# Kernel tuning notes

Hardware: AMD Instinct MI355X
Metric: run time of the kernel (lower is better)

Reference implementation:

```python
import jax, jax.numpy as jnp
import numpy as np

INP = 64   # inplanes
PLN = 64   # planes
LOC = 64   # loc_planes
EPS = 1e-5


def _linear_init(key, fan_in, fan_out):
    # torch nn.Linear default: U(-1/sqrt(fan_in), 1/sqrt(fan_in)) for W and b
    kw, kb = jax.random.split(key)
    bound = 1.0 / np.sqrt(fan_in)
    W = jax.random.uniform(kw, (fan_in, fan_out), jnp.float32, -bound, bound)
    b = jax.random.uniform(kb, (fan_out,), jnp.float32, -bound, bound)
    return W, b


def setup_inputs() -> dict:
    key = jax.random.key(0)
    ks = jax.random.split(key, 8)
    B, N = 8, 4096
    img_fea = jax.random.normal(ks[0], (B, N, INP), jnp.float32)
    loc_fea = jax.random.normal(ks[1], (B, N, LOC), jnp.float32)
    W11, b11 = _linear_init(ks[2], INP + LOC, INP)
    W12, b12 = _linear_init(ks[3], INP, INP)
    W21, b21 = _linear_init(ks[4], INP + LOC, INP)
    W22, b22 = _linear_init(ks[5], INP, INP * PLN)
    W3, b3 = _linear_init(ks[6], PLN, PLN)
    ln_g = jnp.ones((PLN,), jnp.float32)
    ln_b = jnp.zeros((PLN,), jnp.float32)
    return {
        "img_fea": img_fea, "loc_fea": loc_fea,
        "W11": W11, "b11": b11, "W12": W12, "b12": b12,
        "W21": W21, "b21": b21, "W22": W22, "b22": b22,
        "ln_g": ln_g, "ln_b": ln_b, "W3": W3, "b3": b3,
    }


def reference(img_fea, loc_fea, W11, b11, W12, b12, W21, b21, W22, b22,
              ln_g, ln_b, W3, b3):
    B, N, C = img_fea.shape
    cat_fea = jnp.concatenate([img_fea, loc_fea], axis=2)  # [B,N,INP+LOC]
    # branch 1: per-token input vector
    w11 = jax.nn.relu(cat_fea @ W11 + b11)                 # [B,N,INP]
    w12 = w11 @ W12 + b12                                  # [B,N,INP]
    # branch 2: per-token weight matrix generation
    w21 = jax.nn.relu(cat_fea @ W21 + b21)                 # [B,N,INP]
    w22 = (w21 @ W22 + b22).reshape(B, N, INP, PLN)        # [B,N,INP,PLN]
    # batched tiny matvec: (1,INP) @ (INP,PLN) per token
    x = jnp.einsum('bni,bnio->bno', w12, w22)              # [B,N,PLN]
    # LayerNorm over last dim + ReLU
    mu = jnp.mean(x, axis=-1, keepdims=True)
    var = jnp.mean(jnp.square(x - mu), axis=-1, keepdims=True)
    x = (x - mu) * jax.lax.rsqrt(var + EPS) * ln_g + ln_b
    x = jax.nn.relu(x)
    # final linear (no activation)
    return x @ W3 + b3
```

## Files before the change

### kernel.cpp

```cpp
#include <hip/hip_runtime.h>
#include <cstdint>


typedef __bf16 bf16x4 __attribute__((ext_vector_type(4)));
typedef __bf16 bf16x8 __attribute__((ext_vector_type(8)));
typedef float  f32x4  __attribute__((ext_vector_type(4)));

#define MFMA16(A, B, C) __builtin_amdgcn_mfma_f32_16x16x32_bf16(A, B, C, 0, 0, 0)

#define OFF_BT22 0
#define OFF_W11  266240
#define OFF_W21  274432
#define OFF_W12  282624
#define OFF_W3   286720

__global__ __launch_bounds__(256) void prep_kernel(
    const float* __restrict__ W22, const float* __restrict__ b22,
    const float* __restrict__ W11, const float* __restrict__ W21,
    const float* __restrict__ W12, const float* __restrict__ W3,
    __bf16* __restrict__ ws)
{
    __shared__ __bf16 T[64][72];
    const int b = blockIdx.x, tid = threadIdx.x;
    const float* src; long base = 0;
    if (b < 64)       { src = W22 + b * 4096; }
    else if (b == 64) { src = b22; }
    else if (b < 67)  { src = W11 + (b - 65) * 4096; base = OFF_W11 + (b - 65) * 4096; }
    else if (b < 69)  { src = W21 + (b - 67) * 4096; base = OFF_W21 + (b - 67) * 4096; }
    else if (b == 69) { src = W12;                   base = OFF_W12; }
    else              { src = W3;                    base = OFF_W3; }
    #pragma unroll
    for (int it = 0; it < 4; ++it) {
        int u = it * 1024 + tid * 4;
        int r = u >> 6, c = u & 63;
        const float4 v = *(const float4*)(src + u);
        T[r][c] = (__bf16)v.x; T[r][c + 1] = (__bf16)v.y;
        T[r][c + 2] = (__bf16)v.z; T[r][c + 3] = (__bf16)v.w;
    }
    __syncthreads();
    #pragma unroll
    for (int it = 0; it < 2; ++it) {
        int item = it * 256 + tid;
        int q = item >> 6, o = item & 63;
        bf16x8 pk;
        #pragma unroll
        for (int kj = 0; kj < 8; ++kj) pk[kj] = T[q * 8 + kj][o];
        long dstE;
        if (b <= 64) {
            int k8 = (b == 64 ? 512 : b * 8) + q;
            dstE = OFF_BT22 + ((long)(o >> 4) * 520 + k8) * 128 + (o & 15) * 8;
        } else {
            dstE = base + q * 512 + o * 8;
        }
        *(bf16x8*)(ws + dstE) = pk;
    }
}

#define LOADCH(buf, c) do {                                          \
    buf##_0 = *(const bf16x8*)(Bw + ((c)*16 +  0) * 128);            \
    buf##_1 = *(const bf16x8*)(Bw + ((c)*16 +  4) * 128);            \
    buf##_2 = *(const bf16x8*)(Bw + ((c)*16 +  8) * 128);            \
    buf##_3 = *(const bf16x8*)(Bw + ((c)*16 + 12) * 128);            \
} while (0)

#define COMPUTE_J(b0, b1, j) do {                                    \
    f32x4 w4[4];                                                     \
    _Pragma("unroll")                                                \
    for (int mf = 0; mf < 4; ++mf) {                                 \
        bf16x4 wv4 = *(const bf16x4*)(w21T + (j)*68 + mf*16 + quad*4);\
        w4[mf] = __builtin_convertvector(wv4, f32x4);                \
    }                                                                \
    _Pragma("unroll")                                                \
    for (int mf = 0; mf < 4; ++mf) {                                 \
        f32x4 fz = {};                                               \
        f32x4 m = MFMA16(a12[mf][0], b0, fz);                        \
        m       = MFMA16(a12[mf][1], b1, m);                         \
        _Pragma("unroll")                                            \
        for (int r = 0; r < 4; ++r)                                  \
            acc[mf][r] = fmaf(w4[mf][r], m[r], acc[mf][r]);          \
    }                                                                \
} while (0)

#define COMPUTE(buf, c) do {                                         \
    COMPUTE_J(buf##_0, buf##_1, (c)*2);                              \
    COMPUTE_J(buf##_2, buf##_3, (c)*2 + 1);                          \
} while (0)

__global__ __launch_bounds__(256, 2) void main_kernel(
    const float* __restrict__ img, const float* __restrict__ loc,
    const float* __restrict__ b11, const float* __restrict__ b12,
    const float* __restrict__ b21, const float* __restrict__ ln_g,
    const float* __restrict__ ln_b, const float* __restrict__ b3,
    const __bf16* __restrict__ ws, float* __restrict__ out)
{
    __shared__ __align__(1024) char smem[46592];
    __bf16* catL = (__bf16*)smem;
    __bf16* w11L = (__bf16*)(smem + 17408);
    __bf16* w12L = (__bf16*)(smem + 26624);
    __bf16* w21T = (__bf16*)(smem + 35840);
    float2* ps   = (float2*)(smem + 44544);
    __bf16* xL   = w11L;

    const int tid  = threadIdx.x;
    const int wv   = tid >> 6;
    const int lane = tid & 63;
    const int ln   = lane & 15;
    const int quad = lane >> 4;
    const int ob   = wv * 16;
    const long tb  = (long)blockIdx.x * 64;

    const __bf16* Bt22  = ws + OFF_BT22;
    const __bf16* W11bt = ws + OFF_W11;
    const __bf16* W21bt = ws + OFF_W21;
    const __bf16* W12bt = ws + OFF_W12;
    const __bf16* W3bt  = ws + OFF_W3;

    {
        const float* srcs[2] = {img, loc};
        #pragma unroll
        for (int s = 0; s < 2; ++s) {
            const float* src = srcs[s] + tb * 64;
            #pragma unroll
            for (int it = 0; it < 4; ++it) {
                int u = (it * 256 + tid) * 4;
                int t = u >> 6, c = u & 63;
                const float4 v = *(const float4*)(src + u);
                bf16x4 pk = {(__bf16)v.x, (__bf16)v.y, (__bf16)v.z, (__bf16)v.w};
                *(bf16x4*)(catL + t * 136 + s * 64 + c) = pk;
            }
        }
    }
    __syncthreads();

    {
        const int isW21 = wv >> 1;
        const int cb0 = (wv & 1) * 32;
        const __bf16* Wbt = isW21 ? W21bt : W11bt;
        const float* bsel = isW21 ? b21 : b11;
        f32x4 a1[4][2] = {};
        #pragma unroll
        for (int kb = 0; kb < 4; ++kb) {
            bf16x8 af[4];
            #pragma unroll
            for (int mf = 0; mf < 4; ++mf)
                af[mf] = *(const bf16x8*)(catL + (mf*16 + ln)*136 + kb*32 + quad*8);
            #pragma unroll
            for (int nf = 0; nf < 2; ++nf) {
                bf16x8 bw = *(const bf16x8*)(Wbt + ((kb*4 + quad)*64 + cb0 + nf*16 + ln)*8);
                #pragma unroll
                for (int mf = 0; mf < 4; ++mf)
                    a1[mf][nf] = MFMA16(af[mf], bw, a1[mf][nf]);
            }
        }
        if (!isW21) {
            #pragma unroll
            for (int nf = 0; nf < 2; ++nf) {
                int o = cb0 + nf*16 + ln;
                float cb = bsel[o];
                #pragma unroll
                for (int mf = 0; mf < 4; ++mf)
                    #pragma unroll
                    for (int r = 0; r < 4; ++r) {
                        int t = mf*16 + quad*4 + r;
                        float v = a1[mf][nf][r] + cb; v = v > 0.f ? v : 0.f;
                        w11L[t*72 + o] = (__bf16)v;
                    }
            }
        } else {
            #pragma unroll
            for (int nf = 0; nf < 2; ++nf) {
                int o = cb0 + nf*16 + ln;
                float cb = bsel[o];
                #pragma unroll
                for (int mf = 0; mf < 4; ++mf) {
                    bf16x4 pk;
                    #pragma unroll
                    for (int r = 0; r < 4; ++r) {
                        float v = a1[mf][nf][r] + cb; v = v > 0.f ? v : 0.f;
                        pk[r] = (__bf16)v;
                    }
                    *(bf16x4*)(w21T + o*68 + mf*16 + quad*4) = pk;
                }
            }
        }
    }
    __syncthreads();

    {
        float c12 = b12[ob + ln];
        f32x4 a12c[4] = {};
        #pragma unroll
        for (int kb = 0; kb < 2; ++kb) {
            bf16x8 af[4];
            #pragma unroll
            for (int mf = 0; mf < 4; ++mf)
                af[mf] = *(const bf16x8*)(w11L + (mf*16 + ln)*72 + kb*32 + quad*8);
            bf16x8 bw = *(const bf16x8*)(W12bt + ((kb*4 + quad)*64 + ob + ln)*8);
            #pragma unroll
            for (int mf = 0; mf < 4; ++mf)
                a12c[mf] = MFMA16(af[mf], bw, a12c[mf]);
        }
        #pragma unroll
        for (int mf = 0; mf < 4; ++mf)
            #pragma unroll
            for (int r = 0; r < 4; ++r) {
                int t = mf*16 + quad*4 + r;
                w12L[t*72 + ob + ln] = (__bf16)(a12c[mf][r] + c12);
            }
    }
    __syncthreads();

    bf16x8 a12[4][2];
    #pragma unroll
    for (int mf = 0; mf < 4; ++mf)
        #pragma unroll
        for (int sub = 0; sub < 2; ++sub)
            a12[mf][sub] = *(const bf16x8*)(w12L + (mf*16 + ln)*72 + sub*32 + quad*8);

    const __bf16* Bw = Bt22 + ((long)wv * 520 + quad) * 128 + ln * 8;

    bf16x8 B0_0, B0_1, B0_2, B0_3;
    bf16x8 B1_0, B1_1, B1_2, B1_3;
    bf16x8 B2_0, B2_1, B2_2, B2_3;

    f32x4 acc[4] = {};
    LOADCH(B0, 0); LOADCH(B1, 1);
    #pragma unroll 1
    for (int cc = 0; cc < 32; cc += 3) {
        if (cc + 2 < 32) LOADCH(B2, cc + 2);
        COMPUTE(B0, cc);
        if (cc + 3 < 32) LOADCH(B0, cc + 3);
        if (cc + 1 < 32) COMPUTE(B1, cc + 1);
        if (cc + 4 < 32) LOADCH(B1, cc + 4);
        if (cc + 2 < 32) COMPUTE(B2, cc + 2);
    }
    {
        bf16x8 bb0 = *(const bf16x8*)(Bw + (512 + 0) * 128);
        bf16x8 bb1 = *(const bf16x8*)(Bw + (512 + 4) * 128);
        #pragma unroll
        for (int mf = 0; mf < 4; ++mf) {
            acc[mf] = MFMA16(a12[mf][0], bb0, acc[mf]);
            acc[mf] = MFMA16(a12[mf][1], bb1, acc[mf]);
        }
    }

    #pragma unroll
    for (int mf = 0; mf < 4; ++mf)
        #pragma unroll
        for (int r = 0; r < 4; ++r) {
            float v = acc[mf][r];
            float s1 = v, s2 = v*v;
            #pragma unroll
            for (int d = 1; d < 16; d <<= 1) {
                s1 += __shfl_xor(s1, d, 64);
                s2 += __shfl_xor(s2, d, 64);
            }
            if (ln == 0) {
                int t = mf*16 + quad*4 + r;
                ps[t*4 + wv] = make_float2(s1, s2);
            }
        }
    __syncthreads();

    float gv = ln_g[ob + ln], bv = ln_b[ob + ln], b3v = b3[ob + ln];
    #pragma unroll
    for (int mf = 0; mf < 4; ++mf)
        #pragma unroll
        for (int r = 0; r < 4; ++r) {
            int t = mf*16 + quad*4 + r;
            float2 p0 = ps[t*4], p1 = ps[t*4 + 1], p2 = ps[t*4 + 2], p3 = ps[t*4 + 3];
            float mean = (p0.x + p1.x + p2.x + p3.x) * 0.015625f;
            float var  = (p0.y + p1.y + p2.y + p3.y) * 0.015625f - mean * mean;
            float inv  = rsqrtf(var + 1e-5f);
            float v = (acc[mf][r] - mean) * inv * gv + bv;
            v = v > 0.f ? v : 0.f;
            xL[t*72 + ob + ln] = (__bf16)v;
        }
    __syncthreads();

    f32x4 a3[4] = {};
    #pragma unroll
    for (int kb = 0; kb < 2; ++kb) {
        bf16x8 af[4];
        #pragma unroll
        for (int mf = 0; mf < 4; ++mf)
            af[mf] = *(const bf16x8*)(xL + (mf*16 + ln)*72 + kb*32 + quad*8);
        bf16x8 bfr = *(const bf16x8*)(W3bt + ((kb*4 + quad)*64 + ob + ln)*8);
        #pragma unroll
        for (int mf = 0; mf < 4; ++mf)
            a3[mf] = MFMA16(af[mf], bfr, a3[mf]);
    }
    #pragma unroll
    for (int mf = 0; mf < 4; ++mf)
        #pragma unroll
        for (int r = 0; r < 4; ++r) {
            long t = tb + mf*16 + quad*4 + r;
            out[t*64 + ob + ln] = a3[mf][r] + b3v;
        }
}

extern "C" void kernel_launch(void* const* d_in, const int* in_sizes, int n_in,
                              void* d_out, int out_size, void* d_ws, size_t ws_size,
                              hipStream_t stream)
{
    const float* img  = (const float*)d_in[0];
    const float* loc  = (const float*)d_in[1];
    const float* W11  = (const float*)d_in[2];
    const float* b11  = (const float*)d_in[3];
    const float* W12  = (const float*)d_in[4];
    const float* b12  = (const float*)d_in[5];
    const float* W21  = (const float*)d_in[6];
    const float* b21  = (const float*)d_in[7];
    const float* W22  = (const float*)d_in[8];
    const float* b22  = (const float*)d_in[9];
    const float* ln_g = (const float*)d_in[10];
    const float* ln_b = (const float*)d_in[11];
    const float* W3   = (const float*)d_in[12];
    const float* b3   = (const float*)d_in[13];
    __bf16* ws = (__bf16*)d_ws;
    float*  o  = (float*)d_out;

    prep_kernel<<<71, 256, 0, stream>>>(W22, b22, W11, W21, W12, W3, ws);
    main_kernel<<<512, 256, 0, stream>>>(img, loc, b11, b12, b21, ln_g, ln_b, b3, ws, o);
}
```

Baseline: 115.9 us.

## Process 128 tokens per block to halve W22 weight streaming

Each block now handles 128 tokens instead of 64, doubling the M-fragments per wave. Every W22 chunk loaded from global memory is therefore reused across twice as many tokens, and the grid shrinks to 256 blocks. The shared memory layout is reorganized with aliasing so the larger buffers fit in about 70KB. Register pressure rises sharply (a12 and acc arrays double), and with 256 blocks on a 256-CU device occupancy drops to roughly one block per CU, which limits latency hiding.

```diff
diff --git a/kernel.cpp b/kernel.cpp
--- a/kernel.cpp
+++ b/kernel.cpp
@@ -64,14 +64,14 @@
 } while (0)
 
 #define COMPUTE_J(b0, b1, j) do {                                    \
-    f32x4 w4[4];                                                     \
+    f32x4 w4[8];                                                     \
     _Pragma("unroll")                                                \
-    for (int mf = 0; mf < 4; ++mf) {                                 \
-        bf16x4 wv4 = *(const bf16x4*)(w21T + (j)*68 + mf*16 + quad*4);\
+    for (int mf = 0; mf < 8; ++mf) {                                 \
+        bf16x4 wv4 = *(const bf16x4*)(w21T + (j)*132 + mf*16 + quad*4);\
         w4[mf] = __builtin_convertvector(wv4, f32x4);                \
     }                                                                \
     _Pragma("unroll")                                                \
-    for (int mf = 0; mf < 4; ++mf) {                                 \
+    for (int mf = 0; mf < 8; ++mf) {                                 \
         f32x4 fz = {};                                               \
         f32x4 m = MFMA16(a12[mf][0], b0, fz);                        \
         m       = MFMA16(a12[mf][1], b1, m);                         \
@@ -86,20 +86,22 @@
     COMPUTE_J(buf##_2, buf##_3, (c)*2 + 1);                          \
 } while (0)
 
-__global__ __launch_bounds__(256, 2) void main_kernel(
+__global__ __launch_bounds__(256)
+__attribute__((amdgpu_waves_per_eu(2, 2)))
+void main_kernel(
     const float* __restrict__ img, const float* __restrict__ loc,
     const float* __restrict__ b11, const float* __restrict__ b12,
     const float* __restrict__ b21, const float* __restrict__ ln_g,
     const float* __restrict__ ln_b, const float* __restrict__ b3,
     const __bf16* __restrict__ ws, float* __restrict__ out)
 {
-    __shared__ __align__(1024) char smem[46592];
+    __shared__ __align__(1024) char smem[70144];
     __bf16* catL = (__bf16*)smem;
-    __bf16* w11L = (__bf16*)(smem + 17408);
-    __bf16* w12L = (__bf16*)(smem + 26624);
-    __bf16* w21T = (__bf16*)(smem + 35840);
-    float2* ps   = (float2*)(smem + 44544);
+    __bf16* w12L = (__bf16*)smem;
+    float2* ps   = (float2*)(smem + 18432);
+    __bf16* w11L = (__bf16*)(smem + 34816);
     __bf16* xL   = w11L;
+    __bf16* w21T = (__bf16*)(smem + 53248);
 
     const int tid  = threadIdx.x;
     const int wv   = tid >> 6;
@@ -107,7 +109,7 @@
     const int ln   = lane & 15;
     const int quad = lane >> 4;
     const int ob   = wv * 16;
-    const long tb  = (long)blockIdx.x * 64;
+    const long tb  = (long)blockIdx.x * 128;
 
     const __bf16* Bt22  = ws + OFF_BT22;
     const __bf16* W11bt = ws + OFF_W11;
@@ -121,7 +123,7 @@
         for (int s = 0; s < 2; ++s) {
             const float* src = srcs[s] + tb * 64;
             #pragma unroll
-            for (int it = 0; it < 4; ++it) {
+            for (int it = 0; it < 8; ++it) {
                 int u = (it * 256 + tid) * 4;
                 int t = u >> 6, c = u & 63;
                 const float4 v = *(const float4*)(src + u);
@@ -137,19 +139,17 @@
         const int cb0 = (wv & 1) * 32;
         const __bf16* Wbt = isW21 ? W21bt : W11bt;
         const float* bsel = isW21 ? b21 : b11;
-        f32x4 a1[4][2] = {};
+        f32x4 a1[8][2] = {};
         #pragma unroll
         for (int kb = 0; kb < 4; ++kb) {
-            bf16x8 af[4];
-            #pragma unroll
-            for (int mf = 0; mf < 4; ++mf)
-                af[mf] = *(const bf16x8*)(catL + (mf*16 + ln)*136 + kb*32 + quad*8);
             #pragma unroll
             for (int nf = 0; nf < 2; ++nf) {
                 bf16x8 bw = *(const bf16x8*)(Wbt + ((kb*4 + quad)*64 + cb0 + nf*16 + ln)*8);
                 #pragma unroll
-                for (int mf = 0; mf < 4; ++mf)
-                    a1[mf][nf] = MFMA16(af[mf], bw, a1[mf][nf]);
+                for (int mf = 0; mf < 8; ++mf) {
+                    bf16x8 af = *(const bf16x8*)(catL + (mf*16 + ln)*136 + kb*32 + quad*8);
+                    a1[mf][nf] = MFMA16(af, bw, a1[mf][nf]);
+                }
             }
         }
         if (!isW21) {
@@ -158,7 +158,7 @@
                 int o = cb0 + nf*16 + ln;
                 float cb = bsel[o];
                 #pragma unroll
-                for (int mf = 0; mf < 4; ++mf)
+                for (int mf = 0; mf < 8; ++mf)
                     #pragma unroll
                     for (int r = 0; r < 4; ++r) {
                         int t = mf*16 + quad*4 + r;
@@ -172,14 +172,14 @@
                 int o = cb0 + nf*16 + ln;
                 float cb = bsel[o];
                 #pragma unroll
-                for (int mf = 0; mf < 4; ++mf) {
+                for (int mf = 0; mf < 8; ++mf) {
                     bf16x4 pk;
                     #pragma unroll
                     for (int r = 0; r < 4; ++r) {
                         float v = a1[mf][nf][r] + cb; v = v > 0.f ? v : 0.f;
                         pk[r] = (__bf16)v;
                     }
-                    *(bf16x4*)(w21T + o*68 + mf*16 + quad*4) = pk;
+                    *(bf16x4*)(w21T + o*132 + mf*16 + quad*4) = pk;
                 }
             }
         }
@@ -188,20 +188,18 @@
 
     {
         float c12 = b12[ob + ln];
-        f32x4 a12c[4] = {};
+        f32x4 a12c[8] = {};
         #pragma unroll
         for (int kb = 0; kb < 2; ++kb) {
-            bf16x8 af[4];
-            #pragma unroll
-            for (int mf = 0; mf < 4; ++mf)
-                af[mf] = *(const bf16x8*)(w11L + (mf*16 + ln)*72 + kb*32 + quad*8);
             bf16x8 bw = *(const bf16x8*)(W12bt + ((kb*4 + quad)*64 + ob + ln)*8);
             #pragma unroll
-            for (int mf = 0; mf < 4; ++mf)
-                a12c[mf] = MFMA16(af[mf], bw, a12c[mf]);
-        }
-        #pragma unroll
-        for (int mf = 0; mf < 4; ++mf)
+            for (int mf = 0; mf < 8; ++mf) {
+                bf16x8 af = *(const bf16x8*)(w11L + (mf*16 + ln)*72 + kb*32 + quad*8);
+                a12c[mf] = MFMA16(af, bw, a12c[mf]);
+            }
+        }
+        #pragma unroll
+        for (int mf = 0; mf < 8; ++mf)
             #pragma unroll
             for (int r = 0; r < 4; ++r) {
                 int t = mf*16 + quad*4 + r;
@@ -210,9 +208,9 @@
     }
     __syncthreads();
 
-    bf16x8 a12[4][2];
-    #pragma unroll
-    for (int mf = 0; mf < 4; ++mf)
+    bf16x8 a12[8][2];
+    #pragma unroll
+    for (int mf = 0; mf < 8; ++mf)
         #pragma unroll
         for (int sub = 0; sub < 2; ++sub)
             a12[mf][sub] = *(const bf16x8*)(w12L + (mf*16 + ln)*72 + sub*32 + quad*8);
@@ -223,7 +221,7 @@
     bf16x8 B1_0, B1_1, B1_2, B1_3;
     bf16x8 B2_0, B2_1, B2_2, B2_3;
 
-    f32x4 acc[4] = {};
+    f32x4 acc[8] = {};
     LOADCH(B0, 0); LOADCH(B1, 1);
     #pragma unroll 1
     for (int cc = 0; cc < 32; cc += 3) {
@@ -238,14 +236,14 @@
         bf16x8 bb0 = *(const bf16x8*)(Bw + (512 + 0) * 128);
         bf16x8 bb1 = *(const bf16x8*)(Bw + (512 + 4) * 128);
         #pragma unroll
-        for (int mf = 0; mf < 4; ++mf) {
+        for (int mf = 0; mf < 8; ++mf) {
             acc[mf] = MFMA16(a12[mf][0], bb0, acc[mf]);
             acc[mf] = MFMA16(a12[mf][1], bb1, acc[mf]);
         }
     }
 
     #pragma unroll
-    for (int mf = 0; mf < 4; ++mf)
+    for (int mf = 0; mf < 8; ++mf)
         #pragma unroll
         for (int r = 0; r < 4; ++r) {
             float v = acc[mf][r];
@@ -264,7 +262,7 @@
 
     float gv = ln_g[ob + ln], bv = ln_b[ob + ln], b3v = b3[ob + ln];
     #pragma unroll
-    for (int mf = 0; mf < 4; ++mf)
+    for (int mf = 0; mf < 8; ++mf)
         #pragma unroll
         for (int r = 0; r < 4; ++r) {
             int t = mf*16 + quad*4 + r;
@@ -278,20 +276,18 @@
         }
     __syncthreads();
 
-    f32x4 a3[4] = {};
+    f32x4 a3[8] = {};
     #pragma unroll
     for (int kb = 0; kb < 2; ++kb) {
-        bf16x8 af[4];
-        #pragma unroll
-        for (int mf = 0; mf < 4; ++mf)
-            af[mf] = *(const bf16x8*)(xL + (mf*16 + ln)*72 + kb*32 + quad*8);
         bf16x8 bfr = *(const bf16x8*)(W3bt + ((kb*4 + quad)*64 + ob + ln)*8);
         #pragma unroll
-        for (int mf = 0; mf < 4; ++mf)
-            a3[mf] = MFMA16(af[mf], bfr, a3[mf]);
-    }
-    #pragma unroll
-    for (int mf = 0; mf < 4; ++mf)
+        for (int mf = 0; mf < 8; ++mf) {
+            bf16x8 af = *(const bf16x8*)(xL + (mf*16 + ln)*72 + kb*32 + quad*8);
+            a3[mf] = MFMA16(af, bfr, a3[mf]);
+        }
+    }
+    #pragma unroll
+    for (int mf = 0; mf < 8; ++mf)
         #pragma unroll
         for (int r = 0; r < 4; ++r) {
             long t = tb + mf*16 + quad*4 + r;
@@ -321,5 +317,5 @@
     float*  o  = (float*)d_out;
 
     prep_kernel<<<71, 256, 0, stream>>>(W22, b22, W11, W21, W12, W3, ws);
-    main_kernel<<<512, 256, 0, stream>>>(img, loc, b11, b12, b21, ln_g, ln_b, b3, ws, o);
+    main_kernel<<<256, 256, 0, stream>>>(img, loc, b11, b12, b21, ln_g, ln_b, b3, ws, o);
 }
```

Measured after the change: 195.9 us. +69.0%, slower.
